# Performance work log

Hardware: AMD Instinct MI355X
Metric: run time of the kernel (lower is better)

Reference implementation:

```python
import jax, jax.numpy as jnp
import numpy as np

N_NODES = 100000
N_EDGES = 500000
D_IN = 128
D_HID = 256
D_OUT = 1


def mish(x):
    # x * tanh(softplus(x))
    return x * jnp.tanh(jax.nn.softplus(x))


def setup_inputs() -> dict:
    key = jax.random.key(0)
    k1, k2, k3, k4, k5, k6 = jax.random.split(key, 6)
    z = jax.random.normal(k1, (N_NODES, D_IN), dtype=jnp.float32)
    edge = jax.random.randint(k2, (2, N_EDGES), 0, N_NODES, dtype=jnp.int64)
    # PyTorch Linear default init: U(-1/sqrt(fan_in), 1/sqrt(fan_in))
    s1 = 1.0 / np.sqrt(D_IN)
    s2 = 1.0 / np.sqrt(D_HID)
    W1 = jax.random.uniform(k3, (D_HID, D_IN), minval=-s1, maxval=s1, dtype=jnp.float32)
    b1 = jax.random.uniform(k4, (D_HID,), minval=-s1, maxval=s1, dtype=jnp.float32)
    W2 = jax.random.uniform(k5, (D_OUT, D_HID), minval=-s2, maxval=s2, dtype=jnp.float32)
    b2 = jax.random.uniform(k6, (D_OUT,), minval=-s2, maxval=s2, dtype=jnp.float32)
    return {"z": z, "edge": edge, "W1": W1, "b1": b1, "W2": W2, "b2": b2}


def reference(z, edge, W1, b1, W2, b2):
    # gather node pairs and elementwise product: [E, D_IN]
    x = z[edge[0]] * z[edge[1]]
    # fc1 + mish (dropout is identity in eval mode)
    h = mish(jnp.einsum('ed,hd->eh', x, W1) + b1)
    # fc2 + sigmoid -> [E, 1]
    logits = jnp.einsum('eh,oh->eo', h, W2) + b2
    return jax.nn.sigmoid(logits)
```

## Files before the change

### kernel.cpp

```cpp
#include <hip/hip_runtime.h>
#include <hip/hip_bf16.h>
#include <hip/hip_fp16.h>
#include <type_traits>


#define N_NODES 100000
#define N_EDGES 500000
#define D_IN    128
#define D_HID   256
#define PAIRS   (N_EDGES / 32)
#define GRID    512
#define NWAVES  16
#define TOTAL_WAVES (GRID * NWAVES)
#define LDS_ROW 288

#define LOG2E 1.44269504f
#define LN2   0.69314718f
#define XCLMP 28.854f

typedef _Float16 half8  __attribute__((ext_vector_type(8)));
typedef __fp16   fp16x2 __attribute__((ext_vector_type(2)));
typedef __bf16   bf16x8 __attribute__((ext_vector_type(8)));
typedef float    f32x4  __attribute__((ext_vector_type(4)));
typedef float    f32x2  __attribute__((ext_vector_type(2)));

__device__ __forceinline__ unsigned int pkh_u32(float a, float b) {
    fp16x2 r = __builtin_amdgcn_cvt_pkrtz(a, b);
    return __builtin_bit_cast(unsigned int, r);
}
__device__ __forceinline__ unsigned int pkbf_u32(float a, float b) {
    union { __hip_bfloat162 v; unsigned int u; } c;
    c.v = __float22bfloat162_rn(make_float2(a, b));
    return c.u;
}
__device__ __forceinline__ float exp2a(float x) {
    float r; asm("v_exp_f32 %0, %1" : "=v"(r) : "v"(x)); return r;
}
__device__ __forceinline__ float sigf(float x) {
    return __builtin_amdgcn_rcpf(1.0f + __expf(-x));
}

__device__ __forceinline__ void mish2p(f32x2 xs, f32x2 ww, f32x2& dot) {
    f32x2 E;
    E.x = exp2a(fminf(xs.x, XCLMP));
    E.y = exp2a(fminf(xs.y, XCLMP));
    f32x2 num = E * (E + 2.0f);
    f32x2 den = num + 2.0f;
    f32x2 r;
    r.x = __builtin_amdgcn_rcpf(den.x);
    r.y = __builtin_amdgcn_rcpf(den.y);
    f32x2 m = xs * num * r;
    dot += m * ww;
}

__global__ __launch_bounds__(256)
void zcvt_kernel(const float* __restrict__ z, _Float16* __restrict__ zh) {
    const size_t i = (size_t)blockIdx.x * 256 + threadIdx.x;
    const float4 f0 = *reinterpret_cast<const float4*>(z + i * 8);
    const float4 f1 = *reinterpret_cast<const float4*>(z + i * 8 + 4);
    union { half8 h; uint4 u; } o;
    o.h[0] = (_Float16)f0.x; o.h[1] = (_Float16)f0.y;
    o.h[2] = (_Float16)f0.z; o.h[3] = (_Float16)f0.w;
    o.h[4] = (_Float16)f1.x; o.h[5] = (_Float16)f1.y;
    o.h[6] = (_Float16)f1.z; o.h[7] = (_Float16)f1.w;
    *reinterpret_cast<uint4*>(zh + i * 8) = o.u;
}

template <bool USE_H>
__global__ __launch_bounds__(1024, 8)
void edge_mlp_kernel(const float*    __restrict__ z,
                     const _Float16* __restrict__ zh,
                     const int*      __restrict__ edge,
                     const float*    __restrict__ W1,
                     const float*    __restrict__ b1,
                     const float*    __restrict__ W2,
                     const float*    __restrict__ b2,
                     float*          __restrict__ out) {
    using frag_t = std::conditional_t<USE_H, half8, bf16x8>;

    __shared__ __align__(16) char smem[2048 + D_HID * LDS_ROW];

    const int t = threadIdx.x;

    if (t < 256) {
        ((float*)smem)[t]          = b1[t] * LOG2E;
        ((float*)(smem + 1024))[t] = W2[t] * LN2;
    }
    #pragma unroll
    for (int i = 0; i < 4; ++i) {
        const int c    = t + i * 1024;
        const int h    = c >> 4;
        const int slot = c & 15;
        const float* src = W1 + h * D_IN + slot * 8;
        const float4 f0 = *reinterpret_cast<const float4*>(src);
        const float4 f1 = *reinterpret_cast<const float4*>(src + 4);
        uint4 o;
        if constexpr (USE_H) {
            o = make_uint4(pkh_u32(f0.x * LOG2E, f0.y * LOG2E),
                           pkh_u32(f0.z * LOG2E, f0.w * LOG2E),
                           pkh_u32(f1.x * LOG2E, f1.y * LOG2E),
                           pkh_u32(f1.z * LOG2E, f1.w * LOG2E));
        } else {
            o = make_uint4(pkbf_u32(f0.x * LOG2E, f0.y * LOG2E),
                           pkbf_u32(f0.z * LOG2E, f0.w * LOG2E),
                           pkbf_u32(f1.x * LOG2E, f1.y * LOG2E),
                           pkbf_u32(f1.z * LOG2E, f1.w * LOG2E));
        }
        *reinterpret_cast<uint4*>(smem + 2048 + h * LDS_ROW + slot * 16) = o;
    }
    __syncthreads();

    const int wave = t >> 6;
    const int lane = t & 63;
    const int quad = lane >> 4;
    const int nlo  = lane & 15;
    const int gw   = (blockIdx.x << 4) + wave;

    const char*  ldsA  = smem + 2048 + nlo * LDS_ROW + quad * 16;
    const float* ldsB1 = (const float*)(smem + quad * 16);
    const float* ldsW2 = (const float*)(smem + 1024 + quad * 16);
    const float  b2f   = b2[0];
    const int    qoffH = quad * 16;
    const int    qoffF = quad * 32;

    for (int pi = gw; pi < PAIRS; pi += TOTAL_WAVES) {
        const int e0 = pi * 32 + nlo;
        const int u0 = edge[e0],      v0 = edge[N_EDGES + e0];
        const int u1 = edge[e0 + 16], v1 = edge[N_EDGES + e0 + 16];

        frag_t bf0[4], bf1[4];
        if constexpr (USE_H) {
            const char* zb = reinterpret_cast<const char*>(zh);
            const int ou0 = (u0 << 8) + qoffH, ov0 = (v0 << 8) + qoffH;
            const int ou1 = (u1 << 8) + qoffH, ov1 = (v1 << 8) + qoffH;
            #pragma unroll
            for (int ks = 0; ks < 4; ++ks) {
                bf0[ks] = *reinterpret_cast<const half8*>(zb + ou0 + ks * 64) *
                          *reinterpret_cast<const half8*>(zb + ov0 + ks * 64);
                bf1[ks] = *reinterpret_cast<const half8*>(zb + ou1 + ks * 64) *
                          *reinterpret_cast<const half8*>(zb + ov1 + ks * 64);
            }
        } else {
            const char* zb = reinterpret_cast<const char*>(z) + qoffF;
            const char* pu0 = zb + ((size_t)u0 << 9);
            const char* pv0 = zb + ((size_t)v0 << 9);
            const char* pu1 = zb + ((size_t)u1 << 9);
            const char* pv1 = zb + ((size_t)v1 << 9);
            #pragma unroll
            for (int ks = 0; ks < 4; ++ks) {
                float4 a0 = *reinterpret_cast<const float4*>(pu0 + ks * 128);
                float4 a1 = *reinterpret_cast<const float4*>(pu0 + ks * 128 + 16);
                float4 c0 = *reinterpret_cast<const float4*>(pv0 + ks * 128);
                float4 c1 = *reinterpret_cast<const float4*>(pv0 + ks * 128 + 16);
                union { uint4 u; bf16x8 v; } o;
                o.u = make_uint4(pkbf_u32(a0.x*c0.x, a0.y*c0.y),
                                 pkbf_u32(a0.z*c0.z, a0.w*c0.w),
                                 pkbf_u32(a1.x*c1.x, a1.y*c1.y),
                                 pkbf_u32(a1.z*c1.z, a1.w*c1.w));
                bf0[ks] = o.v;
            }
            #pragma unroll
            for (int ks = 0; ks < 4; ++ks) {
                float4 a0 = *reinterpret_cast<const float4*>(pu1 + ks * 128);
                float4 a1 = *reinterpret_cast<const float4*>(pu1 + ks * 128 + 16);
                float4 c0 = *reinterpret_cast<const float4*>(pv1 + ks * 128);
                float4 c1 = *reinterpret_cast<const float4*>(pv1 + ks * 128 + 16);
                union { uint4 u; bf16x8 v; } o;
                o.u = make_uint4(pkbf_u32(a0.x*c0.x, a0.y*c0.y),
                                 pkbf_u32(a0.z*c0.z, a0.w*c0.w),
                                 pkbf_u32(a1.x*c1.x, a1.y*c1.y),
                                 pkbf_u32(a1.z*c1.z, a1.w*c1.w));
                bf1[ks] = o.v;
            }
        }

        f32x2 dot0 = (f32x2){0.f, 0.f}, dot1 = (f32x2){0.f, 0.f};
        #pragma unroll 2
        for (int g = 0; g < 16; ++g) {
            const float4 b1v = *reinterpret_cast<const float4*>(ldsB1 + g * 16);
            f32x4 acc0 = (f32x4){b1v.x, b1v.y, b1v.z, b1v.w};
            f32x4 acc1 = acc0;
            const char* lA = ldsA + g * (16 * LDS_ROW);
            #pragma unroll
            for (int ks = 0; ks < 4; ++ks) {
                frag_t wf = *reinterpret_cast<const frag_t*>(lA + ks * 64);
                if constexpr (USE_H) {
                    acc0 = __builtin_amdgcn_mfma_f32_16x16x32_f16(wf, bf0[ks], acc0, 0, 0, 0);
                    acc1 = __builtin_amdgcn_mfma_f32_16x16x32_f16(wf, bf1[ks], acc1, 0, 0, 0);
                } else {
                    acc0 = __builtin_amdgcn_mfma_f32_16x16x32_bf16(wf, bf0[ks], acc0, 0, 0, 0);
                    acc1 = __builtin_amdgcn_mfma_f32_16x16x32_bf16(wf, bf1[ks], acc1, 0, 0, 0);
                }
            }
            const float4 w2v = *reinterpret_cast<const float4*>(ldsW2 + g * 16);
            const f32x2 wA = (f32x2){w2v.x, w2v.y};
            const f32x2 wB = (f32x2){w2v.z, w2v.w};
            mish2p((f32x2){acc0[0], acc0[1]}, wA, dot0);
            mish2p((f32x2){acc0[2], acc0[3]}, wB, dot0);
            mish2p((f32x2){acc1[0], acc1[1]}, wA, dot1);
            mish2p((f32x2){acc1[2], acc1[3]}, wB, dot1);
        }

        float l0 = dot0.x + dot0.y;
        float l1 = dot1.x + dot1.y;
        l0 += __shfl_xor(l0, 16);  l0 += __shfl_xor(l0, 32);
        l1 += __shfl_xor(l1, 16);  l1 += __shfl_xor(l1, 32);
        if (quad == 0) {
            out[pi * 32 + nlo]      = sigf(l0 + b2f);
            out[pi * 32 + 16 + nlo] = sigf(l1 + b2f);
        }
    }
}

extern "C" void kernel_launch(void* const* d_in, const int* in_sizes, int n_in,
                              void* d_out, int out_size, void* d_ws, size_t ws_size,
                              hipStream_t stream) {
    const float* z    = (const float*)d_in[0];
    const int*   edge = (const int*)d_in[1];
    const float* W1   = (const float*)d_in[2];
    const float* b1   = (const float*)d_in[3];
    const float* W2   = (const float*)d_in[4];
    const float* b2   = (const float*)d_in[5];
    float* out = (float*)d_out;

    const size_t zh_bytes = (size_t)N_NODES * D_IN * sizeof(_Float16);
    if (d_ws != nullptr && ws_size >= zh_bytes) {
        _Float16* zh = (_Float16*)d_ws;
        zcvt_kernel<<<dim3(N_NODES * D_IN / 8 / 256), dim3(256), 0, stream>>>(z, zh);
        edge_mlp_kernel<true><<<dim3(GRID), dim3(1024), 0, stream>>>(
            z, zh, edge, W1, b1, W2, b2, out);
    } else {
        edge_mlp_kernel<false><<<dim3(GRID), dim3(1024), 0, stream>>>(
            z, nullptr, edge, W1, b1, W2, b2, out);
    }
}
```

Before: 164.8 us.

## Software-pipeline node-row gathers and halve block size to 512 threads

Adds register double-buffering for the fp16 path: node rows for the next pair are gathered while the current pair's MFMA work runs, and edge indices are fetched two iterations ahead. Blocks shrink from 1024 to 512 threads (8 waves) with launch bounds of 4 blocks per CU, so the grid has half as many total waves. The goal is to hide gather latency behind compute, at the cost of more VGPRs per thread for the prefetch buffers and fewer resident waves.

```diff
diff --git a/kernel.cpp b/kernel.cpp
--- a/kernel.cpp
+++ b/kernel.cpp
@@ -10,7 +10,7 @@
 #define D_HID   256
 #define PAIRS   (N_EDGES / 32)
 #define GRID    512
-#define NWAVES  16
+#define NWAVES  8
 #define TOTAL_WAVES (GRID * NWAVES)
 #define LDS_ROW 288
 
@@ -67,7 +67,7 @@
 }
 
 template <bool USE_H>
-__global__ __launch_bounds__(1024, 8)
+__global__ __launch_bounds__(512, 4)
 void edge_mlp_kernel(const float*    __restrict__ z,
                      const _Float16* __restrict__ zh,
                      const int*      __restrict__ edge,
@@ -87,8 +87,8 @@
         ((float*)(smem + 1024))[t] = W2[t] * LN2;
     }
     #pragma unroll
-    for (int i = 0; i < 4; ++i) {
-        const int c    = t + i * 1024;
+    for (int i = 0; i < 8; ++i) {
+        const int c    = t + i * 512;
         const int h    = c >> 4;
         const int slot = c & 15;
         const float* src = W1 + h * D_IN + slot * 8;
@@ -114,7 +114,7 @@
     const int lane = t & 63;
     const int quad = lane >> 4;
     const int nlo  = lane & 15;
-    const int gw   = (blockIdx.x << 4) + wave;
+    const int gw   = (blockIdx.x << 3) + wave;
 
     const char*  ldsA  = smem + 2048 + nlo * LDS_ROW + quad * 16;
     const float* ldsB1 = (const float*)(smem + quad * 16);
@@ -123,24 +123,62 @@
     const int    qoffH = quad * 16;
     const int    qoffF = quad * 32;
 
+    half8 ru0[4], rv0[4], ru1[4], rv1[4];
+    int   nu0 = 0, nv0 = 0, nu1 = 0, nv1 = 0;
+    if constexpr (USE_H) {
+        const char* zb = reinterpret_cast<const char*>(zh);
+        {
+            const int e = gw * 32 + nlo;
+            const int ou0 = (edge[e] << 8) + qoffH;
+            const int ov0 = (edge[N_EDGES + e] << 8) + qoffH;
+            const int ou1 = (edge[e + 16] << 8) + qoffH;
+            const int ov1 = (edge[N_EDGES + e + 16] << 8) + qoffH;
+            #pragma unroll
+            for (int ks = 0; ks < 4; ++ks) {
+                ru0[ks] = *reinterpret_cast<const half8*>(zb + ou0 + ks * 64);
+                rv0[ks] = *reinterpret_cast<const half8*>(zb + ov0 + ks * 64);
+                ru1[ks] = *reinterpret_cast<const half8*>(zb + ou1 + ks * 64);
+                rv1[ks] = *reinterpret_cast<const half8*>(zb + ov1 + ks * 64);
+            }
+        }
+        {
+            const int pn = min(gw + TOTAL_WAVES, PAIRS - 1);
+            const int e  = pn * 32 + nlo;
+            nu0 = (edge[e] << 8) + qoffH;
+            nv0 = (edge[N_EDGES + e] << 8) + qoffH;
+            nu1 = (edge[e + 16] << 8) + qoffH;
+            nv1 = (edge[N_EDGES + e + 16] << 8) + qoffH;
+        }
+    }
+
     for (int pi = gw; pi < PAIRS; pi += TOTAL_WAVES) {
-        const int e0 = pi * 32 + nlo;
-        const int u0 = edge[e0],      v0 = edge[N_EDGES + e0];
-        const int u1 = edge[e0 + 16], v1 = edge[N_EDGES + e0 + 16];
-
         frag_t bf0[4], bf1[4];
         if constexpr (USE_H) {
+            #pragma unroll
+            for (int ks = 0; ks < 4; ++ks) {
+                bf0[ks] = ru0[ks] * rv0[ks];
+                bf1[ks] = ru1[ks] * rv1[ks];
+            }
             const char* zb = reinterpret_cast<const char*>(zh);
-            const int ou0 = (u0 << 8) + qoffH, ov0 = (v0 << 8) + qoffH;
-            const int ou1 = (u1 << 8) + qoffH, ov1 = (v1 << 8) + qoffH;
-            #pragma unroll
-            for (int ks = 0; ks < 4; ++ks) {
-                bf0[ks] = *reinterpret_cast<const half8*>(zb + ou0 + ks * 64) *
-                          *reinterpret_cast<const half8*>(zb + ov0 + ks * 64);
-                bf1[ks] = *reinterpret_cast<const half8*>(zb + ou1 + ks * 64) *
-                          *reinterpret_cast<const half8*>(zb + ov1 + ks * 64);
+            #pragma unroll
+            for (int ks = 0; ks < 4; ++ks) {
+                ru0[ks] = *reinterpret_cast<const half8*>(zb + nu0 + ks * 64);
+                rv0[ks] = *reinterpret_cast<const half8*>(zb + nv0 + ks * 64);
+                ru1[ks] = *reinterpret_cast<const half8*>(zb + nu1 + ks * 64);
+                rv1[ks] = *reinterpret_cast<const half8*>(zb + nv1 + ks * 64);
+            }
+            {
+                const int p2 = min(pi + 2 * TOTAL_WAVES, PAIRS - 1);
+                const int e  = p2 * 32 + nlo;
+                nu0 = (edge[e] << 8) + qoffH;
+                nv0 = (edge[N_EDGES + e] << 8) + qoffH;
+                nu1 = (edge[e + 16] << 8) + qoffH;
+                nv1 = (edge[N_EDGES + e + 16] << 8) + qoffH;
             }
         } else {
+            const int e0 = pi * 32 + nlo;
+            const int u0 = edge[e0],      v0 = edge[N_EDGES + e0];
+            const int u1 = edge[e0 + 16], v1 = edge[N_EDGES + e0 + 16];
             const char* zb = reinterpret_cast<const char*>(z) + qoffF;
             const char* pu0 = zb + ((size_t)u0 << 9);
             const char* pv0 = zb + ((size_t)v0 << 9);
@@ -158,14 +196,10 @@
                                  pkbf_u32(a1.x*c1.x, a1.y*c1.y),
                                  pkbf_u32(a1.z*c1.z, a1.w*c1.w));
                 bf0[ks] = o.v;
-            }
-            #pragma unroll
-            for (int ks = 0; ks < 4; ++ks) {
-                float4 a0 = *reinterpret_cast<const float4*>(pu1 + ks * 128);
-                float4 a1 = *reinterpret_cast<const float4*>(pu1 + ks * 128 + 16);
-                float4 c0 = *reinterpret_cast<const float4*>(pv1 + ks * 128);
-                float4 c1 = *reinterpret_cast<const float4*>(pv1 + ks * 128 + 16);
-                union { uint4 u; bf16x8 v; } o;
+                a0 = *reinterpret_cast<const float4*>(pu1 + ks * 128);
+                a1 = *reinterpret_cast<const float4*>(pu1 + ks * 128 + 16);
+                c0 = *reinterpret_cast<const float4*>(pv1 + ks * 128);
+                c1 = *reinterpret_cast<const float4*>(pv1 + ks * 128 + 16);
                 o.u = make_uint4(pkbf_u32(a0.x*c0.x, a0.y*c0.y),
                                  pkbf_u32(a0.z*c0.z, a0.w*c0.w),
                                  pkbf_u32(a1.x*c1.x, a1.y*c1.y),
@@ -227,10 +261,10 @@
     if (d_ws != nullptr && ws_size >= zh_bytes) {
         _Float16* zh = (_Float16*)d_ws;
         zcvt_kernel<<<dim3(N_NODES * D_IN / 8 / 256), dim3(256), 0, stream>>>(z, zh);
-        edge_mlp_kernel<true><<<dim3(GRID), dim3(1024), 0, stream>>>(
+        edge_mlp_kernel<true><<<dim3(GRID), dim3(512), 0, stream>>>(
             z, zh, edge, W1, b1, W2, b2, out);
     } else {
-        edge_mlp_kernel<false><<<dim3(GRID), dim3(1024), 0, stream>>>(
+        edge_mlp_kernel<false><<<dim3(GRID), dim3(512), 0, stream>>>(
             z, nullptr, edge, W1, b1, W2, b2, out);
     }
 }
```

After: 172.3 us. +4.6%, slower.
